# Kernel tuning notes

Hardware: AMD Instinct MI355X
Metric: run time of the kernel (lower is better)

The kernel has to match this reference:

```python
import jax, jax.numpy as jnp
import numpy as np

B_, L_, DM_, DS_, DC_, EXP_ = 2, 2048, 1024, 16, 4, 2
DI_ = EXP_ * DM_

def setup_inputs() -> dict:
    key = jax.random.key(0)
    ks = jax.random.split(key, 8)
    rn = lambda k, shape, s: (jax.random.normal(k, shape, dtype=jnp.float32) * s)
    return {
        "x": rn(ks[0], (B_, L_, DM_), 1.0),
        "in_proj_w": rn(ks[1], (2 * DI_, DM_), 0.02),
        "conv_w": rn(ks[2], (DI_, 1, DC_), 0.1),
        "conv_b": jnp.zeros((DI_,), dtype=jnp.float32),
        "x_proj_w": rn(ks[3], (2 * DS_ + 1, DI_), 0.02),
        "dt_proj_w": rn(ks[4], (DI_, 1), 0.02),
        "dt_proj_b": jnp.full((DI_,), -2.0, dtype=jnp.float32),
        "A_log": rn(ks[5], (DI_, DS_), 1.0),
        "D": jnp.ones((DI_,), dtype=jnp.float32),
        "out_proj_w": rn(ks[6], (DM_, DI_), 0.02),
    }


def reference(x, in_proj_w, conv_w, conv_b, x_proj_w, dt_proj_w, dt_proj_b, A_log, D, out_proj_w):
    b, l, dm = x.shape
    di, ds = A_log.shape
    dc = conv_w.shape[-1]

    # in_proj -> split into u (ssm stream) and z (gate)
    xz = x @ in_proj_w.T                      # (b, l, 2*di)
    u, z = xz[..., :di], xz[..., di:]

    # causal depthwise conv1d (torch pads both sides then slices [:l] == left pad only)
    uc = jnp.transpose(u, (0, 2, 1))          # (b, di, l)
    uc = jax.lax.conv_general_dilated(
        uc, conv_w, window_strides=(1,), padding=[(dc - 1, 0)],
        feature_group_count=di, dimension_numbers=("NCH", "OIH", "NCH"))
    uc = uc + conv_b[None, :, None]
    u = jnp.transpose(uc, (0, 2, 1)) * jax.nn.silu(z)   # (b, l, di)

    # input-dependent SSM params
    proj = u @ x_proj_w.T                     # (b, l, 2*ds + 1)
    delta = proj[..., :1]                     # (b, l, 1)
    Bm = proj[..., 1:1 + ds]                  # (b, l, ds)
    Cm = proj[..., 1 + ds:]                   # (b, l, ds)
    delta = jax.nn.softplus(delta @ dt_proj_w.T + dt_proj_b)  # (b, l, di)

    A = -jnp.exp(A_log)                       # (di, ds)

    def step(h, inp):
        ut, dt, Bt, Ct = inp                  # (b,di) (b,di) (b,ds) (b,ds)
        dte = jnp.exp(dt)                     # faithful to source: exp(softplus(...))
        A_bar = jnp.exp(A[None] * dte[..., None])          # (b, di, ds)
        h = A_bar * h + (Bt[:, None, :] * dte[..., None]) * ut[..., None]
        yt = jnp.einsum("bis,bs->bi", h, Ct) + D * ut
        return h, yt

    h0 = jnp.zeros((b, di, ds), dtype=x.dtype)
    xs = (jnp.transpose(u, (1, 0, 2)), jnp.transpose(delta, (1, 0, 2)),
          jnp.transpose(Bm, (1, 0, 2)), jnp.transpose(Cm, (1, 0, 2)))
    _, ys = jax.lax.scan(step, h0, xs)        # ys: (l, b, di)
    y = jnp.transpose(ys, (1, 0, 2))          # (b, l, di)
    return y @ out_proj_w.T                   # (b, l, dm)
```

## Files before the change

### kernel.cpp

```cpp
#include <hip/hip_runtime.h>
#include <hip/hip_bf16.h>
#include <cstddef>
#include <cstdint>

#define B_N 2
#define L_N 2048
#define DM_N 1024
#define DS_N 16
#define DI_N 2048
#define NTOK (B_N * L_N)
#define NPROJ 33
#define NPJ 36
#define NC 64
#define CL (L_N / NC)
#define XKC 8
#define XKCL (DI_N / XKC)

typedef __attribute__((ext_vector_type(8))) short short8v;
typedef __attribute__((ext_vector_type(4))) float f32x4;
typedef __attribute__((address_space(1))) void av1;
typedef __attribute__((address_space(3))) void av3;

__device__ __forceinline__ void gload16(const void* g, void* l) {
  __builtin_amdgcn_global_load_lds((av1*)g, (av3*)l, 16, 0, 0);
}

__device__ __forceinline__ unsigned short f2bf_rn(float f) {
  uint32_t u = __float_as_uint(f);
  uint32_t r = (u + 0x7fffu + ((u >> 16) & 1u)) >> 16;
  return (unsigned short)r;
}
__device__ __forceinline__ float bf2f(unsigned short h) {
  return __uint_as_float((uint32_t)h << 16);
}

__global__ __launch_bounds__(256) void split_pack_kernel(
    const float* __restrict__ src, uint32_t* __restrict__ dst, int n8) {
  int idx = blockIdx.x * 256 + threadIdx.x;
  if (idx >= n8) return;
  const float4* s = (const float4*)src + (size_t)idx * 2;
  float4 v0 = s[0], v1 = s[1];
  float f[8] = {v0.x, v0.y, v0.z, v0.w, v1.x, v1.y, v1.z, v1.w};
  uint32_t hi[4], lo[4];
#pragma unroll
  for (int j = 0; j < 4; ++j) {
    unsigned short h0 = f2bf_rn(f[2 * j]);
    unsigned short h1 = f2bf_rn(f[2 * j + 1]);
    unsigned short l0 = f2bf_rn(f[2 * j] - bf2f(h0));
    unsigned short l1 = f2bf_rn(f[2 * j + 1] - bf2f(h1));
    hi[j] = (uint32_t)h0 | ((uint32_t)h1 << 16);
    lo[j] = (uint32_t)l0 | ((uint32_t)l1 << 16);
  }
  uint4* d = (uint4*)dst + (size_t)idx * 2;
  d[0] = make_uint4(hi[0], hi[1], hi[2], hi[3]);
  d[1] = make_uint4(lo[0], lo[1], lo[2], lo[3]);
}

__global__ __launch_bounds__(256) void gemm_pk_nt(
    const char* __restrict__ Apk, const char* __restrict__ Bpk,
    float* __restrict__ C, int N, int K4, int gx) {
  __shared__ __align__(16) char lds[32768];
  const int tid = threadIdx.x;
  const int lane = tid & 63;
  const int wave = tid >> 6;

  const int nwg = gridDim.x;
  const int cpx = nwg >> 3;
  const int bid = blockIdx.x;
  const int wg = (bid & 7) * cpx + (bid >> 3);
  const int bx = wg % gx;
  const int by = wg / gx;
  const int m0 = by * 128, n0 = bx * 128;

  const int wr = wave >> 1, wc = wave & 1;

  const char* gbase = (wave & 2) ? Bpk : Apk;
  const int rowbase = ((wave & 2) ? n0 : m0) + (wave & 1) * 64;
  const int rloc = lane >> 3;
  const int sslot = (lane & 7) ^ rloc;
  const char* gsrc = gbase + (size_t)(rowbase + rloc) * K4 + sslot * 16;
  const size_t cstride = (size_t)8 * K4;
  char* ldst = lds + wave * 8192 + lane * 16;

  f32x4 acc[4][4] = {};
  const int fr = lane & 15;
  const int fg = lane >> 4;
  const int sA = ((fg * 2) ^ (fr & 7)) * 16;
  const int abase = (wr * 64 + fr) * 128 + sA;
  const int bbase = 16384 + (wc * 64 + fr) * 128 + sA;

  for (int kt4 = 0; kt4 < K4; kt4 += 128) {
#pragma unroll
    for (int c = 0; c < 8; ++c)
      gload16(gsrc + c * cstride + kt4, ldst + c * 1024);
    __syncthreads();

    short8v afh[4], afl[4], bfh[4], bfl[4];
#pragma unroll
    for (int m = 0; m < 4; ++m) {
      int a = abase + m * 2048;
      afh[m] = *(const short8v*)(lds + a);
      afl[m] = *(const short8v*)(lds + (a ^ 16));
    }
#pragma unroll
    for (int n = 0; n < 4; ++n) {
      int b = bbase + n * 2048;
      bfh[n] = *(const short8v*)(lds + b);
      bfl[n] = *(const short8v*)(lds + (b ^ 16));
    }
#pragma unroll
    for (int m = 0; m < 4; ++m) {
#pragma unroll
      for (int n = 0; n < 4; ++n) {
        asm("v_mfma_f32_16x16x32_bf16 %0, %1, %2, %0"
            : "+v"(acc[m][n]) : "v"(afh[m]), "v"(bfh[n]));
        asm("v_mfma_f32_16x16x32_bf16 %0, %1, %2, %0"
            : "+v"(acc[m][n]) : "v"(afh[m]), "v"(bfl[n]));
        asm("v_mfma_f32_16x16x32_bf16 %0, %1, %2, %0"
            : "+v"(acc[m][n]) : "v"(afl[m]), "v"(bfh[n]));
      }
    }
    __syncthreads();
  }

#pragma unroll
  for (int m = 0; m < 4; ++m) {
#pragma unroll
    for (int n = 0; n < 4; ++n) {
#pragma unroll
      for (int q = 0; q < 4; ++q) {
        int row = m0 + wr * 64 + m * 16 + fg * 4 + q;
        int col = n0 + wc * 64 + n * 16 + fr;
        C[(size_t)row * N + col] = acc[m][n][q];
      }
    }
  }
}

__global__ __launch_bounds__(256) void conv_silu_kernel(
    const float* __restrict__ xz, const float* __restrict__ cw,
    const float* __restrict__ cb, float* __restrict__ u2) {
  size_t idx = (size_t)blockIdx.x * 256 + threadIdx.x;
  if (idx >= (size_t)NTOK * DI_N) return;
  int i = (int)(idx & (DI_N - 1));
  int n = (int)(idx >> 11);
  int l = n & (L_N - 1);
  const float* base = xz + (size_t)n * (2 * DI_N) + i;
  const float4 w = *(const float4*)&cw[i * 4];
  float acc = fmaf(w.w, base[0], cb[i]);
  if (l >= 1) acc = fmaf(w.z, base[-(ptrdiff_t)(2 * DI_N)], acc);
  if (l >= 2) acc = fmaf(w.y, base[-(ptrdiff_t)(4 * DI_N)], acc);
  if (l >= 3) acc = fmaf(w.x, base[-(ptrdiff_t)(6 * DI_N)], acc);
  float z = base[DI_N];
  float sil = z / (1.f + __expf(-z));
  u2[(size_t)n * DI_N + i] = acc * sil;
}

__global__ __launch_bounds__(256) void xproj_part_kernel(
    const float* __restrict__ u2, const float* __restrict__ xw,
    float* __restrict__ part) {
  __shared__ float uS[16][257];
  __shared__ float wS[33][257];
  const int tid = threadIdx.x;
  const int kc = blockIdx.x & (XKC - 1);
  const int rb = blockIdx.x >> 3;
  const int row0 = rb * 16;
  const int k0 = kc * XKCL;

#pragma unroll
  for (int it = 0; it < 4; ++it) {
    int slot = tid + it * 256;
    int r = slot >> 6;
    int kq = (slot & 63) << 2;
    float4 v = *(const float4*)&u2[(size_t)(row0 + r) * DI_N + k0 + kq];
    uS[r][kq] = v.x; uS[r][kq + 1] = v.y;
    uS[r][kq + 2] = v.z; uS[r][kq + 3] = v.w;
  }
#pragma unroll
  for (int it = 0; it < 9; ++it) {
    int slot = tid + it * 256;
    if (slot < 33 * 64) {
      int c = slot >> 6;
      int kq = (slot & 63) << 2;
      float4 v = *(const float4*)&xw[(size_t)c * DI_N + k0 + kq];
      wS[c][kq] = v.x; wS[c][kq + 1] = v.y;
      wS[c][kq + 2] = v.z; wS[c][kq + 3] = v.w;
    }
  }
  __syncthreads();

  const int r = tid & 15;
  const int cg = tid >> 4;
  const int c0 = cg * 3;
  const int rc0 = c0 > 32 ? 32 : c0;
  const int rc1 = c0 + 1 > 32 ? 32 : c0 + 1;
  const int rc2 = c0 + 2 > 32 ? 32 : c0 + 2;
  float a0 = 0.f, a1 = 0.f, a2 = 0.f;
#pragma unroll 4
  for (int k = 0; k < XKCL; ++k) {
    float uv = uS[r][k];
    a0 = fmaf(uv, wS[rc0][k], a0);
    a1 = fmaf(uv, wS[rc1][k], a1);
    a2 = fmaf(uv, wS[rc2][k], a2);
  }
  size_t base = (size_t)kc * (NTOK * NPJ) + (size_t)(row0 + r) * NPJ;
  if (c0 < NPROJ)     part[base + (c0 == 0 ? 0 : c0 + 3)] = a0;
  if (c0 + 1 < NPROJ) part[base + c0 + 4] = a1;
  if (c0 + 2 < NPROJ) part[base + c0 + 5] = a2;
}

__global__ __launch_bounds__(256) void xproj_reduce_kernel(
    const float* __restrict__ part, float* __restrict__ proj) {
  int idx = blockIdx.x * 256 + threadIdx.x;
  float s = 0.f;
#pragma unroll
  for (int kc = 0; kc < XKC; ++kc)
    s += part[(size_t)kc * (NTOK * NPJ) + idx];
  proj[idx] = s;
}

__global__ __launch_bounds__(256) void scan_pass1_kernel(
    const float* __restrict__ u2, const float* __restrict__ pj,
    const float* __restrict__ dtw, const float* __restrict__ dtb,
    const float* __restrict__ A_log,
    float* __restrict__ carryH, float* __restrict__ sdteO) {
  __shared__ float pS[CL][20];
  const int tid = threadIdx.x;
  const int bid = blockIdx.x;
  const int ib = bid & 7;
  const int c = (bid >> 3) & (NC - 1);
  const int b = bid >> 9;
  const int i = ib * 256 + tid;
  const int l0 = c * CL;
  const float LOG2E = 1.4426950408889634f;

  if (tid < CL * 5) {
    int row = tid / 5, j = tid % 5;
    float4 v = *(const float4*)&pj[((size_t)b * L_N + l0 + row) * NPJ + j * 4];
    *(float4*)&pS[row][j * 4] = v;
  }

  float A2[16];
#pragma unroll
  for (int q = 0; q < 4; ++q) {
    float4 v = *(const float4*)&A_log[i * DS_N + q * 4];
    A2[q * 4 + 0] = -__expf(v.x) * LOG2E;
    A2[q * 4 + 1] = -__expf(v.y) * LOG2E;
    A2[q * 4 + 2] = -__expf(v.z) * LOG2E;
    A2[q * 4 + 3] = -__expf(v.w) * LOG2E;
  }
  const float wl = dtw[i] * LOG2E;
  const float bl = dtb[i] * LOG2E;
  const float* un = u2 + ((size_t)b * L_N + l0) * DI_N + i;
  __syncthreads();

  float h[16] = {};
  float sdte = 0.f;
  float ucur = un[0];
#pragma unroll 2
  for (int l = 0; l < CL; ++l) {
    float unext = (l + 1 < CL) ? un[(size_t)(l + 1) * DI_N] : 0.f;
    float d0 = pS[l][0];
    float4 B0 = *(const float4*)&pS[l][4];
    float4 B1 = *(const float4*)&pS[l][8];
    float4 B2 = *(const float4*)&pS[l][12];
    float4 B3 = *(const float4*)&pS[l][16];
    float dte = 1.f + exp2f(fmaf(d0, wl, bl));
    float du = dte * ucur;
    sdte += dte;
    float Bv[16] = {B0.x, B0.y, B0.z, B0.w, B1.x, B1.y, B1.z, B1.w,
                    B2.x, B2.y, B2.z, B2.w, B3.x, B3.y, B3.z, B3.w};
#pragma unroll
    for (int s = 0; s < 16; ++s) {
      float a = exp2f(A2[s] * dte);
      h[s] = fmaf(a, h[s], Bv[s] * du);
    }
    ucur = unext;
  }
  size_t cbase = (((size_t)c * B_N + b) * DI_N + i) * DS_N;
#pragma unroll
  for (int q = 0; q < 4; ++q) {
    float4 hv = {h[q * 4], h[q * 4 + 1], h[q * 4 + 2], h[q * 4 + 3]};
    *(float4*)&carryH[cbase + q * 4] = hv;
  }
  sdteO[((size_t)c * B_N + b) * DI_N + i] = sdte;
}

__global__ __launch_bounds__(256) void scan_fixup_kernel(
    float* __restrict__ carryH, const float* __restrict__ sdte,
    const float* __restrict__ A_log) {
  const int q = blockIdx.x * 256 + threadIdx.x;
  const int s = q & 15;
  const int i = (q >> 4) & (DI_N - 1);
  const float LOG2E = 1.4426950408889634f;
  const float A2 = -__expf(A_log[i * DS_N + s]) * LOG2E;
  float h = 0.f;
#pragma unroll 8
  for (int c = 0; c < NC; ++c) {
    size_t idx = (size_t)c * (B_N * DI_N * DS_N) + q;
    float Hc = carryH[idx];
    float sd = sdte[(size_t)c * (B_N * DI_N) + (q >> 4)];
    carryH[idx] = h;
    h = fmaf(exp2f(A2 * sd), h, Hc);
  }
}

__global__ __launch_bounds__(256) void scan_pass2_kernel(
    const float* __restrict__ u2, const float* __restrict__ pj,
    const float* __restrict__ dtw, const float* __restrict__ dtb,
    const float* __restrict__ A_log, const float* __restrict__ Dp,
    const float* __restrict__ carryH, char* __restrict__ ypk) {
  __shared__ float pS[CL][36];
  const int tid = threadIdx.x;
  const int bid = blockIdx.x;
  const int ib = bid & 7;
  const int c = (bid >> 3) & (NC - 1);
  const int b = bid >> 9;
  const int i = ib * 256 + tid;
  const int l0 = c * CL;
  const float LOG2E = 1.4426950408889634f;

#pragma unroll
  for (int it = 0; it < 2; ++it) {
    int slot = tid + it * 256;
    if (slot < CL * 9) {
      int row = slot / 9, j = slot % 9;
      float4 v = *(const float4*)&pj[((size_t)b * L_N + l0 + row) * NPJ + j * 4];
      *(float4*)&pS[row][j * 4] = v;
    }
  }

  float A2[16];
#pragma unroll
  for (int q = 0; q < 4; ++q) {
    float4 v = *(const float4*)&A_log[i * DS_N + q * 4];
    A2[q * 4 + 0] = -__expf(v.x) * LOG2E;
    A2[q * 4 + 1] = -__expf(v.y) * LOG2E;
    A2[q * 4 + 2] = -__expf(v.z) * LOG2E;
    A2[q * 4 + 3] = -__expf(v.w) * LOG2E;
  }
  const float wl = dtw[i] * LOG2E;
  const float bl = dtb[i] * LOG2E;
  const float Dd = Dp[i];

  float h[16];
  size_t cbase = (((size_t)c * B_N + b) * DI_N + i) * DS_N;
#pragma unroll
  for (int q = 0; q < 4; ++q) {
    float4 hv = *(const float4*)&carryH[cbase + q * 4];
    h[q * 4] = hv.x; h[q * 4 + 1] = hv.y;
    h[q * 4 + 2] = hv.z; h[q * 4 + 3] = hv.w;
  }

  const float* un = u2 + ((size_t)b * L_N + l0) * DI_N + i;
  char* yb = ypk + ((size_t)b * L_N + l0) * (DI_N * 4) + (i >> 3) * 32 + (i & 7) * 2;
  __syncthreads();

  float ucur = un[0];
#pragma unroll 2
  for (int l = 0; l < CL; ++l) {
    float unext = (l + 1 < CL) ? un[(size_t)(l + 1) * DI_N] : 0.f;
    float d0 = pS[l][0];
    float4 B0 = *(const float4*)&pS[l][4];
    float4 B1 = *(const float4*)&pS[l][8];
    float4 B2 = *(const float4*)&pS[l][12];
    float4 B3 = *(const float4*)&pS[l][16];
    float4 C0 = *(const float4*)&pS[l][20];
    float4 C1 = *(const float4*)&pS[l][24];
    float4 C2 = *(const float4*)&pS[l][28];
    float4 C3 = *(const float4*)&pS[l][32];
    float dte = 1.f + exp2f(fmaf(d0, wl, bl));
    float du = dte * ucur;
    float Bv[16] = {B0.x, B0.y, B0.z, B0.w, B1.x, B1.y, B1.z, B1.w,
                    B2.x, B2.y, B2.z, B2.w, B3.x, B3.y, B3.z, B3.w};
    float Cv[16] = {C0.x, C0.y, C0.z, C0.w, C1.x, C1.y, C1.z, C1.w,
                    C2.x, C2.y, C2.z, C2.w, C3.x, C3.y, C3.z, C3.w};
    float y = Dd * ucur;
#pragma unroll
    for (int s = 0; s < 16; ++s) {
      float a = exp2f(A2[s] * dte);
      h[s] = fmaf(a, h[s], Bv[s] * du);
      y = fmaf(h[s], Cv[s], y);
    }
    unsigned short hh = f2bf_rn(y);
    char* q = yb + (size_t)l * (DI_N * 4);
    *(unsigned short*)q = hh;
    *(unsigned short*)(q + 16) = f2bf_rn(y - bf2f(hh));
    ucur = unext;
  }
}

extern "C" void kernel_launch(void* const* d_in, const int* in_sizes, int n_in,
                              void* d_out, int out_size, void* d_ws, size_t ws_size,
                              hipStream_t stream) {
  const float* x          = (const float*)d_in[0];
  const float* in_proj_w  = (const float*)d_in[1];
  const float* conv_w     = (const float*)d_in[2];
  const float* conv_b     = (const float*)d_in[3];
  const float* x_proj_w   = (const float*)d_in[4];
  const float* dt_proj_w  = (const float*)d_in[5];
  const float* dt_proj_b  = (const float*)d_in[6];
  const float* A_log      = (const float*)d_in[7];
  const float* Dp         = (const float*)d_in[8];
  const float* out_proj_w = (const float*)d_in[9];
  float* out = (float*)d_out;

  char* ws = (char*)d_ws;
  float* xz = (float*)ws;
  float* u2 = (float*)(ws + (size_t)NTOK * 2 * DI_N * 4);

  char* x_pk  = (char*)u2;
  char* w1_pk = x_pk + (size_t)NTOK * DM_N * 4;

  char*  y_pk   = ws;
  float* carryH = (float*)(ws + 33554432);
  float* sdte   = (float*)(ws + 50331648);
  char*  w2_pk  = ws + 51380224;
  float* xpart  = (float*)(ws + 59768832);
  float* proj36 = (float*)(ws + 64487424);

  {
    int n8 = NTOK * DM_N / 8;
    split_pack_kernel<<<n8 / 256, 256, 0, stream>>>(x, (uint32_t*)x_pk, n8);
    split_pack_kernel<<<n8 / 256, 256, 0, stream>>>(in_proj_w, (uint32_t*)w1_pk, n8);
  }
  gemm_pk_nt<<<1024, 256, 0, stream>>>(x_pk, w1_pk, xz, 2 * DI_N, DM_N * 4, 32);
  {
    int nblk = (int)(((size_t)NTOK * DI_N + 255) / 256);
    conv_silu_kernel<<<nblk, 256, 0, stream>>>(xz, conv_w, conv_b, u2);
  }
  {
    int n8 = DM_N * DI_N / 8;
    split_pack_kernel<<<n8 / 256, 256, 0, stream>>>(out_proj_w, (uint32_t*)w2_pk, n8);
  }
  {
    xproj_part_kernel<<<(NTOK / 16) * XKC, 256, 0, stream>>>(u2, x_proj_w, xpart);
    xproj_reduce_kernel<<<(NTOK * NPJ) / 256, 256, 0, stream>>>(xpart, proj36);
  }
  {
    int nblk = B_N * NC * (DI_N / 256);
    scan_pass1_kernel<<<nblk, 256, 0, stream>>>(u2, proj36, dt_proj_w, dt_proj_b,
                                                A_log, carryH, sdte);
    scan_fixup_kernel<<<(B_N * DI_N * DS_N) / 256, 256, 0, stream>>>(carryH, sdte,
                                                                     A_log);
    scan_pass2_kernel<<<nblk, 256, 0, stream>>>(u2, proj36, dt_proj_w, dt_proj_b,
                                                A_log, Dp, carryH, y_pk);
  }
  gemm_pk_nt<<<256, 256, 0, stream>>>(y_pk, w2_pk, out, DM_N, DI_N * 4, 8);
}
```

Before: 369.8 us.

## Swizzle GEMM LDS layout, vectorize conv-silu, add split-K scaffolding

Adds an extra row-parity XOR to the GEMM's LDS swizzle, applied on both the global-to-LDS load addresses and the fragment reads, to reduce bank conflicts. Rewrites the causal conv+SiLU kernel to process four channels per thread with float4 loads and stores. Adds split-K parameters to the GEMM, left disabled, and zeroes padding columns in the x_proj partials. The swizzle must stay consistent between writes and reads, or results will be corrupted.

```diff
diff --git a/kernel.cpp b/kernel.cpp
--- a/kernel.cpp
+++ b/kernel.cpp
@@ -58,7 +58,8 @@
 
 __global__ __launch_bounds__(256) void gemm_pk_nt(
     const char* __restrict__ Apk, const char* __restrict__ Bpk,
-    float* __restrict__ C, int N, int K4, int gx) {
+    float* __restrict__ C, int N, int K4, int gx,
+    int kshift, int K4half, size_t cstride) {
   __shared__ __align__(16) char lds[32768];
   const int tid = threadIdx.x;
   const int lane = tid & 63;
@@ -68,8 +69,10 @@
   const int cpx = nwg >> 3;
   const int bid = blockIdx.x;
   const int wg = (bid & 7) * cpx + (bid >> 3);
-  const int bx = wg % gx;
-  const int by = wg / gx;
+  const int kc = wg & ((1 << kshift) - 1);
+  const int tile = wg >> kshift;
+  const int bx = tile % gx;
+  const int by = tile / gx;
   const int m0 = by * 128, n0 = bx * 128;
 
   const int wr = wave >> 1, wc = wave & 1;
@@ -79,20 +82,24 @@
   const int rloc = lane >> 3;
   const int sslot = (lane & 7) ^ rloc;
   const char* gsrc = gbase + (size_t)(rowbase + rloc) * K4 + sslot * 16;
-  const size_t cstride = (size_t)8 * K4;
+  const size_t rstride = (size_t)8 * K4;
   char* ldst = lds + wave * 8192 + lane * 16;
 
   f32x4 acc[4][4] = {};
   const int fr = lane & 15;
   const int fg = lane >> 4;
-  const int sA = ((fg * 2) ^ (fr & 7)) * 16;
+  const int sA = ((fg * 2) ^ (fr & 7) ^ ((fr >> 3) & 1)) * 16;
   const int abase = (wr * 64 + fr) * 128 + sA;
   const int bbase = 16384 + (wc * 64 + fr) * 128 + sA;
 
-  for (int kt4 = 0; kt4 < K4; kt4 += 128) {
-#pragma unroll
-    for (int c = 0; c < 8; ++c)
-      gload16(gsrc + c * cstride + kt4, ldst + c * 1024);
+  const int kt4b = kc * K4half;
+  const int kt4e = kt4b + K4half;
+  for (int kt4 = kt4b; kt4 < kt4e; kt4 += 128) {
+#pragma unroll
+    for (int c = 0; c < 8; ++c) {
+      const char* p = (const char*)((uintptr_t)(gsrc + c * rstride) ^ ((c & 1) << 4));
+      gload16(p + kt4, ldst + c * 1024);
+    }
     __syncthreads();
 
     short8v afh[4], afl[4], bfh[4], bfl[4];
@@ -123,6 +130,7 @@
     __syncthreads();
   }
 
+  float* Cout = C + (size_t)kc * cstride;
 #pragma unroll
   for (int m = 0; m < 4; ++m) {
 #pragma unroll
@@ -131,7 +139,7 @@
       for (int q = 0; q < 4; ++q) {
         int row = m0 + wr * 64 + m * 16 + fg * 4 + q;
         int col = n0 + wc * 64 + n * 16 + fr;
-        C[(size_t)row * N + col] = acc[m][n][q];
+        Cout[(size_t)row * N + col] = acc[m][n][q];
       }
     }
   }
@@ -140,20 +148,33 @@
 __global__ __launch_bounds__(256) void conv_silu_kernel(
     const float* __restrict__ xz, const float* __restrict__ cw,
     const float* __restrict__ cb, float* __restrict__ u2) {
-  size_t idx = (size_t)blockIdx.x * 256 + threadIdx.x;
-  if (idx >= (size_t)NTOK * DI_N) return;
-  int i = (int)(idx & (DI_N - 1));
-  int n = (int)(idx >> 11);
+  int idx = blockIdx.x * 256 + threadIdx.x;
+  int i4 = idx & (DI_N / 4 - 1);
+  int n = idx >> 9;
+  int i = i4 << 2;
   int l = n & (L_N - 1);
   const float* base = xz + (size_t)n * (2 * DI_N) + i;
-  const float4 w = *(const float4*)&cw[i * 4];
-  float acc = fmaf(w.w, base[0], cb[i]);
-  if (l >= 1) acc = fmaf(w.z, base[-(ptrdiff_t)(2 * DI_N)], acc);
-  if (l >= 2) acc = fmaf(w.y, base[-(ptrdiff_t)(4 * DI_N)], acc);
-  if (l >= 3) acc = fmaf(w.x, base[-(ptrdiff_t)(6 * DI_N)], acc);
-  float z = base[DI_N];
-  float sil = z / (1.f + __expf(-z));
-  u2[(size_t)n * DI_N + i] = acc * sil;
+  float4 zero = {0.f, 0.f, 0.f, 0.f};
+  float4 u0 = *(const float4*)base;
+  float4 u1 = (l >= 1) ? *(const float4*)(base - 2 * DI_N) : zero;
+  float4 um2 = (l >= 2) ? *(const float4*)(base - 4 * DI_N) : zero;
+  float4 um3 = (l >= 3) ? *(const float4*)(base - 6 * DI_N) : zero;
+  float4 z = *(const float4*)(base + DI_N);
+  float4 bia = *(const float4*)&cb[i];
+  float4 w0 = *(const float4*)&cw[i * 4];
+  float4 w1 = *(const float4*)&cw[i * 4 + 4];
+  float4 w2 = *(const float4*)&cw[i * 4 + 8];
+  float4 w3 = *(const float4*)&cw[i * 4 + 12];
+  float4 r;
+  r.x = fmaf(w0.w, u0.x, fmaf(w0.z, u1.x, fmaf(w0.y, um2.x, fmaf(w0.x, um3.x, bia.x))));
+  r.y = fmaf(w1.w, u0.y, fmaf(w1.z, u1.y, fmaf(w1.y, um2.y, fmaf(w1.x, um3.y, bia.y))));
+  r.z = fmaf(w2.w, u0.z, fmaf(w2.z, u1.z, fmaf(w2.y, um2.z, fmaf(w2.x, um3.z, bia.z))));
+  r.w = fmaf(w3.w, u0.w, fmaf(w3.z, u1.w, fmaf(w3.y, um2.w, fmaf(w3.x, um3.w, bia.w))));
+  r.x *= z.x / (1.f + __expf(-z.x));
+  r.y *= z.y / (1.f + __expf(-z.y));
+  r.z *= z.z / (1.f + __expf(-z.z));
+  r.w *= z.w / (1.f + __expf(-z.w));
+  *(float4*)&u2[(size_t)n * DI_N + i] = r;
 }
 
 __global__ __launch_bounds__(256) void xproj_part_kernel(
@@ -207,6 +228,9 @@
   if (c0 < NPROJ)     part[base + (c0 == 0 ? 0 : c0 + 3)] = a0;
   if (c0 + 1 < NPROJ) part[base + c0 + 4] = a1;
   if (c0 + 2 < NPROJ) part[base + c0 + 5] = a2;
+  if (cg == 11) {
+    part[base + 1] = 0.f; part[base + 2] = 0.f; part[base + 3] = 0.f;
+  }
 }
 
 __global__ __launch_bounds__(256) void xproj_reduce_kernel(
@@ -424,11 +448,10 @@
     split_pack_kernel<<<n8 / 256, 256, 0, stream>>>(x, (uint32_t*)x_pk, n8);
     split_pack_kernel<<<n8 / 256, 256, 0, stream>>>(in_proj_w, (uint32_t*)w1_pk, n8);
   }
-  gemm_pk_nt<<<1024, 256, 0, stream>>>(x_pk, w1_pk, xz, 2 * DI_N, DM_N * 4, 32);
-  {
-    int nblk = (int)(((size_t)NTOK * DI_N + 255) / 256);
-    conv_silu_kernel<<<nblk, 256, 0, stream>>>(xz, conv_w, conv_b, u2);
-  }
+  gemm_pk_nt<<<1024, 256, 0, stream>>>(x_pk, w1_pk, xz, 2 * DI_N, DM_N * 4, 32,
+                                       0, DM_N * 4, 0);
+  conv_silu_kernel<<<(NTOK * DI_N / 4) / 256, 256, 0, stream>>>(xz, conv_w,
+                                                                conv_b, u2);
   {
     int n8 = DM_N * DI_N / 8;
     split_pack_kernel<<<n8 / 256, 256, 0, stream>>>(out_proj_w, (uint32_t*)w2_pk, n8);
@@ -446,5 +469,6 @@
     scan_pass2_kernel<<<nblk, 256, 0, stream>>>(u2, proj36, dt_proj_w, dt_proj_b,
                                                 A_log, Dp, carryH, y_pk);
   }
-  gemm_pk_nt<<<256, 256, 0, stream>>>(y_pk, w2_pk, out, DM_N, DI_N * 4, 8);
-}
+  gemm_pk_nt<<<256, 256, 0, stream>>>(y_pk, w2_pk, out, DM_N, DI_N * 4, 8,
+                                      0, DI_N * 4, 0);
+}
```

Result: no change. 371.5 us (+0.5%).
